# Performance work log

Measured on AMD Instinct MI355X. Metric: run time of the kernel, lower is better.

The kernel has to match this reference:

```python
import jax, jax.numpy as jnp
import numpy as np

N, VW, DW, VP, DP, H, M = 1024, 50000, 300, 50, 100, 512, 256


def _run_dir(x, Wih, Whh, b, reverse):
    # Single-direction LSTM over [n, in] -> [n, H]. PyTorch gate order i,f,g,o.
    Hh = Whh.shape[1]
    def step(carry, xt):
        h, c = carry
        z = xt @ Wih.T + h @ Whh.T + b  # [4H]
        i, f, g, o = jnp.split(z, 4, axis=-1)
        c = jax.nn.sigmoid(f) * c + jax.nn.sigmoid(i) * jnp.tanh(g)
        h = jax.nn.sigmoid(o) * jnp.tanh(c)
        return (h, c), h
    init = (jnp.zeros((Hh,), x.dtype), jnp.zeros((Hh,), x.dtype))
    _, hs = jax.lax.scan(step, init, x, reverse=reverse)
    return hs


def setup_inputs() -> dict:
    key = jax.random.key(0)
    ks = jax.random.split(key, 24)
    s = 0.05  # small init to keep tanh/sigmoid unsaturated
    d = {
        "word_idx": jax.random.randint(ks[0], (N,), 0, VW, dtype=jnp.int32),
        "pos_idx": jax.random.randint(ks[1], (N,), 0, VP, dtype=jnp.int32),
        "word_emb": jax.random.normal(ks[2], (VW, DW), jnp.float32) * s,
        "pos_emb": jax.random.normal(ks[3], (VP, DP), jnp.float32) * s,
        "wih0f": jax.random.normal(ks[4], (4 * H, DW + DP), jnp.float32) * s,
        "whh0f": jax.random.normal(ks[5], (4 * H, H), jnp.float32) * s,
        "b0f": jax.random.normal(ks[6], (4 * H,), jnp.float32) * s,
        "wih0r": jax.random.normal(ks[7], (4 * H, DW + DP), jnp.float32) * s,
        "whh0r": jax.random.normal(ks[8], (4 * H, H), jnp.float32) * s,
        "b0r": jax.random.normal(ks[9], (4 * H,), jnp.float32) * s,
        "wih1f": jax.random.normal(ks[10], (4 * H, 2 * H), jnp.float32) * s,
        "whh1f": jax.random.normal(ks[11], (4 * H, H), jnp.float32) * s,
        "b1f": jax.random.normal(ks[12], (4 * H,), jnp.float32) * s,
        "wih1r": jax.random.normal(ks[13], (4 * H, 2 * H), jnp.float32) * s,
        "whh1r": jax.random.normal(ks[14], (4 * H, H), jnp.float32) * s,
        "b1r": jax.random.normal(ks[15], (4 * H,), jnp.float32) * s,
        "W1": jax.random.normal(ks[16], (M, 4 * H), jnp.float32) * s,
        "bmlp1": jax.random.normal(ks[17], (M,), jnp.float32) * s,
        "w2": jax.random.normal(ks[18], (1, M), jnp.float32) * s,
        "b2": jax.random.normal(ks[19], (1,), jnp.float32) * s,
    }
    return d


def reference(word_idx, pos_idx, word_emb, pos_emb,
              wih0f, whh0f, b0f, wih0r, whh0r, b0r,
              wih1f, whh1f, b1f, wih1r, whh1r, b1r,
              W1, bmlp1, w2, b2):
    # Embed words + pos, concat -> [n, 400]
    x = jnp.concatenate([word_emb[word_idx], pos_emb[pos_idx]], axis=1)
    # 2-layer bidirectional LSTM encoder (batch of 1 squeezed away, as in the module)
    h0 = jnp.concatenate([_run_dir(x, wih0f, whh0f, b0f, False),
                          _run_dir(x, wih0r, whh0r, b0r, True)], axis=1)   # [n, 2H]
    h1 = jnp.concatenate([_run_dir(h0, wih1f, whh1f, b1f, False),
                          _run_dir(h0, wih1r, whh1r, b1r, True)], axis=1)  # [n, 2H]
    # Pairwise MLP score: MLP(concat(h_i, h_j)). Split W1 into head/dep halves so the
    # big GEMM is done once per token instead of once per pair (same math).
    twoH = h1.shape[1]
    a = h1 @ W1[:, :twoH].T            # [n, M], contribution of h_i
    bpart = h1 @ W1[:, twoH:].T        # [n, M], contribution of h_j
    hidden = jnp.tanh(a[:, None, :] + bpart[None, :, :] + bmlp1)  # [n, n, M]
    scores = hidden @ w2[0] + b2[0]    # [n, n]
    return scores
```

## Files before the change

### kernel.cpp

```cpp
#include <hip/hip_runtime.h>
#include <hip/hip_bf16.h>

#define HID   512
#define SEQ   1024
#define GATES 2048

__device__ __forceinline__ float sigm(float x) {
    return 1.f / (1.f + __expf(-x));
}
__device__ __forceinline__ float tanh_fast(float x) {
    float ax = fabsf(x);
    float e  = __expf(-2.f * ax);
    float t  = (1.f - e) * __builtin_amdgcn_rcpf(1.f + e);
    return copysignf(t, x);
}
__device__ __forceinline__ float bcast(float v, int l) {
    return __uint_as_float((unsigned)__builtin_amdgcn_readlane((int)__float_as_uint(v), l));
}

__global__ void embed_kernel(const int* __restrict__ wi, const int* __restrict__ pi,
                             const float* __restrict__ we, const float* __restrict__ pe,
                             float* __restrict__ x) {
    int i = blockIdx.x;
    int t = threadIdx.x;
    const float* w = we + (size_t)wi[i] * 300;
    const float* p = pe + (size_t)pi[i] * 100;
    float* xo = x + (size_t)i * 400;
    for (int c = t; c < 300; c += 128) xo[c]       = w[c];
    for (int c = t; c < 100; c += 128) xo[300 + c] = p[c];
}

__global__ __launch_bounds__(256)
void gemm_bias2(const float* __restrict__ A,
                const float* __restrict__ B0, const float* __restrict__ bias0, float* __restrict__ C0,
                const float* __restrict__ B1, const float* __restrict__ bias1, float* __restrict__ C1,
                int M, int N, int K, int lda, int ldb, int ldc) {
    const float* B    = blockIdx.z ? B1    : B0;
    const float* bias = blockIdx.z ? bias1 : bias0;
    float*       C    = blockIdx.z ? C1    : C0;

    __shared__ __align__(16) float As[16 * 132];
    __shared__ __align__(16) float Bs[16 * 68];
    const int tid  = threadIdx.x;
    const int bn   = blockIdx.x, bm = blockIdx.y;
    const int tj   = tid & 15, ti = tid >> 4;
    const int arow = tid >> 1;
    const int ak8  = (tid & 1) * 8;
    const int brow = tid >> 2;
    const int bk4  = (tid & 3) * 4;
    float acc[8][4] = {};

    for (int kt = 0; kt < K; kt += 16) {
        float4 a0 = *(const float4*)(A + (size_t)(bm * 128 + arow) * lda + kt + ak8);
        float4 a1 = *(const float4*)(A + (size_t)(bm * 128 + arow) * lda + kt + ak8 + 4);
        float4 bv = *(const float4*)(B + (size_t)(bn * 64 + brow) * ldb + kt + bk4);
        As[(ak8 + 0) * 132 + arow] = a0.x; As[(ak8 + 1) * 132 + arow] = a0.y;
        As[(ak8 + 2) * 132 + arow] = a0.z; As[(ak8 + 3) * 132 + arow] = a0.w;
        As[(ak8 + 4) * 132 + arow] = a1.x; As[(ak8 + 5) * 132 + arow] = a1.y;
        As[(ak8 + 6) * 132 + arow] = a1.z; As[(ak8 + 7) * 132 + arow] = a1.w;
        Bs[(bk4 + 0) * 68 + brow] = bv.x; Bs[(bk4 + 1) * 68 + brow] = bv.y;
        Bs[(bk4 + 2) * 68 + brow] = bv.z; Bs[(bk4 + 3) * 68 + brow] = bv.w;
        __syncthreads();
        #pragma unroll
        for (int k = 0; k < 16; ++k) {
            float4 x0 = *(const float4*)&As[k * 132 + ti * 8];
            float4 x1 = *(const float4*)&As[k * 132 + ti * 8 + 4];
            float4 b4 = *(const float4*)&Bs[k * 68 + tj * 4];
            const float av[8] = {x0.x, x0.y, x0.z, x0.w, x1.x, x1.y, x1.z, x1.w};
            #pragma unroll
            for (int i = 0; i < 8; ++i) {
                acc[i][0] = fmaf(av[i], b4.x, acc[i][0]);
                acc[i][1] = fmaf(av[i], b4.y, acc[i][1]);
                acc[i][2] = fmaf(av[i], b4.z, acc[i][2]);
                acc[i][3] = fmaf(av[i], b4.w, acc[i][3]);
            }
        }
        __syncthreads();
    }
    const int n0 = bn * 64 + tj * 4;
    float bb0 = 0.f, bb1 = 0.f, bb2 = 0.f, bb3 = 0.f;
    if (bias) { bb0 = bias[n0]; bb1 = bias[n0 + 1]; bb2 = bias[n0 + 2]; bb3 = bias[n0 + 3]; }
    #pragma unroll
    for (int i = 0; i < 8; ++i) {
        float4 o;
        o.x = acc[i][0] + bb0; o.y = acc[i][1] + bb1;
        o.z = acc[i][2] + bb2; o.w = acc[i][3] + bb3;
        *(float4*)(C + (size_t)(bm * 128 + ti * 8 + i) * ldc + n0) = o;
    }
}

__global__ __launch_bounds__(576)
void lstm_layer(const float* __restrict__ Zf, const float* __restrict__ Zr,
                const float* __restrict__ WhhF, const float* __restrict__ WhhR,
                unsigned long long* __restrict__ Hpair,
                float* __restrict__ Hout,
                unsigned tagBase) {
    const int dir = blockIdx.x >> 5;
    const int wg  = blockIdx.x & 31;
    const float* __restrict__ Z   = dir ? Zr   : Zf;
    const float* __restrict__ Whh = dir ? WhhR : WhhF;
    const int colOff = dir ? HID : 0;

    const int tid  = threadIdx.x;
    const int wave = tid >> 6;
    const int lane = tid & 63;
    const int g    = lane >> 4;
    const int jj   = lane & 15;
    const int grow = g * HID + wg * 16 + jj;

    __shared__ float part[2][8 * 65];

    if (wave == 0) {
        float cval = 0.f;
        float zin = Z[(size_t)(dir ? (SEQ - 1) : 0) * GATES + grow];
        for (int s = 0; s < SEQ; ++s) {
            const int t = dir ? (SEQ - 1 - s) : s;
            float znxt = 0.f;
            if (s + 1 < SEQ) {
                const int tn = dir ? (SEQ - 2 - s) : (s + 1);
                znxt = Z[(size_t)tn * GATES + grow];
            }
            __syncthreads();
            const float* pp = part[s & 1];
            float r = zin;
            #pragma unroll
            for (int c = 0; c < 8; ++c) r += pp[c * 65 + lane];
            float nl = (g == 2) ? tanh_fast(r) : sigm(r);
            float ig = __shfl(nl, jj);
            float fg = __shfl(nl, 16 + jj);
            float gg = __shfl(nl, 32 + jj);
            float og = __shfl(nl, 48 + jj);
            if (lane < 16) {
                cval = fg * cval + ig * gg;
                float hv = og * tanh_fast(cval);
                const size_t oidx = (size_t)t * (2 * HID) + colOff + wg * 16 + lane;
                unsigned long long pk = ((unsigned long long)(tagBase + (unsigned)s) << 32)
                                      | (unsigned long long)__float_as_uint(hv);
                __hip_atomic_store(Hpair + oidx, pk, __ATOMIC_RELAXED, __HIP_MEMORY_SCOPE_AGENT);
                Hout[oidx] = hv;
            }
            zin = znxt;
        }
    } else {
        const int kc = wave - 1;
        float w[64];
        {
            const float4* wp = (const float4*)(Whh + (size_t)grow * HID + kc * 64);
            #pragma unroll
            for (int q = 0; q < 16; ++q) {
                float4 v = wp[q];
                w[4 * q] = v.x; w[4 * q + 1] = v.y; w[4 * q + 2] = v.z; w[4 * q + 3] = v.w;
            }
        }
        for (int s = 0; s < SEQ; ++s) {
            const int t = dir ? (SEQ - 1 - s) : s;
            float acc = 0.f;
            if (s > 0) {
                const int tp = dir ? (t + 1) : (t - 1);
                const unsigned expTag = tagBase + (unsigned)s - 1u;
                const unsigned long long* hp =
                    Hpair + (size_t)tp * (2 * HID) + colOff + kc * 64 + lane;
                unsigned long long va, vb, v;
                va = __hip_atomic_load(hp, __ATOMIC_RELAXED, __HIP_MEMORY_SCOPE_AGENT);
                for (;;) {
                    vb = __hip_atomic_load(hp, __ATOMIC_RELAXED, __HIP_MEMORY_SCOPE_AGENT);
                    if (__all((unsigned)(va >> 32) == expTag)) { v = va; break; }
                    va = __hip_atomic_load(hp, __ATOMIC_RELAXED, __HIP_MEMORY_SCOPE_AGENT);
                    if (__all((unsigned)(vb >> 32) == expTag)) { v = vb; break; }
                }
                float hv = __uint_as_float((unsigned)v);
                float a0 = 0.f, a1 = 0.f, a2 = 0.f, a3 = 0.f;
                #pragma unroll
                for (int m = 0; m < 64; m += 4) {
                    a0 = fmaf(w[m + 0], bcast(hv, m + 0), a0);
                    a1 = fmaf(w[m + 1], bcast(hv, m + 1), a1);
                    a2 = fmaf(w[m + 2], bcast(hv, m + 2), a2);
                    a3 = fmaf(w[m + 3], bcast(hv, m + 3), a3);
                }
                acc = (a0 + a1) + (a2 + a3);
            }
            part[s & 1][kc * 65 + lane] = acc;
            __syncthreads();
        }
    }
}

__global__ __launch_bounds__(256)
void pairwise_kernel(const float* __restrict__ Ah, const float* __restrict__ Bd,
                     const float* __restrict__ w2, const float* __restrict__ b2,
                     float* __restrict__ out) {
    __shared__ __align__(16) float at[16 * 260];
    __shared__ __align__(16) float bt[16 * 260];
    __shared__ __align__(16) float wl[256];
    const int tid = threadIdx.x;
    const int i0 = blockIdx.y * 16, j0 = blockIdx.x * 16;
    for (int u = tid; u < 16 * 256; u += 256) {
        int r = u >> 8, m = u & 255;
        at[r * 260 + m] = Ah[(size_t)(i0 + r) * 256 + m];
        bt[r * 260 + m] = Bd[(size_t)(j0 + r) * 256 + m];
    }
    wl[tid] = w2[tid];
    __syncthreads();
    const int tj = tid & 15, ti = tid >> 4;
    float acc = b2[0];
    #pragma unroll 2
    for (int m = 0; m < 256; m += 4) {
        float4 a4 = *(const float4*)&at[ti * 260 + m];
        float4 b4 = *(const float4*)&bt[tj * 260 + m];
        float4 w4 = *(const float4*)&wl[m];
        acc += tanh_fast(a4.x + b4.x) * w4.x;
        acc += tanh_fast(a4.y + b4.y) * w4.y;
        acc += tanh_fast(a4.z + b4.z) * w4.z;
        acc += tanh_fast(a4.w + b4.w) * w4.w;
    }
    out[(size_t)(i0 + ti) * 1024 + (j0 + tj)] = acc;
}

extern "C" void kernel_launch(void* const* d_in, const int* in_sizes, int n_in,
                              void* d_out, int out_size, void* d_ws, size_t ws_size,
                              hipStream_t stream) {
    const int*   wi    = (const int*)  d_in[0];
    const int*   pi    = (const int*)  d_in[1];
    const float* we    = (const float*)d_in[2];
    const float* pe    = (const float*)d_in[3];
    const float* wih0f = (const float*)d_in[4];
    const float* whh0f = (const float*)d_in[5];
    const float* b0f   = (const float*)d_in[6];
    const float* wih0r = (const float*)d_in[7];
    const float* whh0r = (const float*)d_in[8];
    const float* b0r   = (const float*)d_in[9];
    const float* wih1f = (const float*)d_in[10];
    const float* whh1f = (const float*)d_in[11];
    const float* b1f   = (const float*)d_in[12];
    const float* wih1r = (const float*)d_in[13];
    const float* whh1r = (const float*)d_in[14];
    const float* b1r   = (const float*)d_in[15];
    const float* W1    = (const float*)d_in[16];
    const float* bmlp1 = (const float*)d_in[17];
    const float* w2    = (const float*)d_in[18];
    const float* b2    = (const float*)d_in[19];
    float* out = (float*)d_out;

    char* wsb = (char*)d_ws;
    float* x  = (float*)(wsb + 512);
    float* zA = x  + (size_t)1024 * 400;
    float* zB = zA + (size_t)1024 * 2048;
    float* h0 = zB + (size_t)1024 * 2048;
    float* h1 = h0 + (size_t)1024 * 1024;
    float* aH = h1 + (size_t)1024 * 1024;
    float* bD = aH + (size_t)1024 * 256;
    unsigned long long* Hpair = (unsigned long long*)(bD + (size_t)1024 * 256);

    embed_kernel<<<dim3(1024), dim3(128), 0, stream>>>(wi, pi, we, pe, x);

    gemm_bias2<<<dim3(32, 8, 2), dim3(256), 0, stream>>>(
        x, wih0f, b0f, zA, wih0r, b0r, zB, 1024, 2048, 400, 400, 400, 2048);

    lstm_layer<<<dim3(64), dim3(576), 0, stream>>>(zA, zB, whh0f, whh0r, Hpair, h0, 1u);

    gemm_bias2<<<dim3(32, 8, 2), dim3(256), 0, stream>>>(
        h0, wih1f, b1f, zA, wih1r, b1r, zB, 1024, 2048, 1024, 1024, 1024, 2048);

    lstm_layer<<<dim3(64), dim3(576), 0, stream>>>(zA, zB, whh1f, whh1r, Hpair, h1, 8192u);

    gemm_bias2<<<dim3(4, 8, 2), dim3(256), 0, stream>>>(
        h1, W1, bmlp1, aH, W1 + 1024, nullptr, bD, 1024, 256, 1024, 1024, 2048, 256);

    pairwise_kernel<<<dim3(64, 64), dim3(256), 0, stream>>>(aH, bD, w2, b2, out);
}
```

Baseline: 3.392 ms.

## Enlarge GEMM and pairwise tiles, pipeline LSTM spin-wait loads

The input-projection GEMM tile grows from 128x64 to 128x128, so each thread computes an 8x8 block and loads less shared memory per FMA. The pairwise scoring kernel moves to 32x32 tiles with 2x2 outputs per thread and an XOR-swizzled shared layout, reads w2 straight from global memory, and shares each A/B load across four tanh evaluations. The LSTM spin-wait now keeps three loads in flight as a rolling window instead of alternating two. The trade-off is higher register pressure and fewer blocks for the small GEMM, while the LSTM recurrence, which probably dominates runtime, is mostly unchanged.

```diff
diff --git a/kernel.cpp b/kernel.cpp
--- a/kernel.cpp
+++ b/kernel.cpp
@@ -31,61 +31,66 @@
 }
 
 __global__ __launch_bounds__(256)
-void gemm_bias2(const float* __restrict__ A,
-                const float* __restrict__ B0, const float* __restrict__ bias0, float* __restrict__ C0,
-                const float* __restrict__ B1, const float* __restrict__ bias1, float* __restrict__ C1,
-                int M, int N, int K, int lda, int ldb, int ldc) {
+void gemm128(const float* __restrict__ A,
+             const float* __restrict__ B0, const float* __restrict__ bias0, float* __restrict__ C0,
+             const float* __restrict__ B1, const float* __restrict__ bias1, float* __restrict__ C1,
+             int K, int lda, int ldb, int ldc) {
     const float* B    = blockIdx.z ? B1    : B0;
     const float* bias = blockIdx.z ? bias1 : bias0;
     float*       C    = blockIdx.z ? C1    : C0;
 
     __shared__ __align__(16) float As[16 * 132];
-    __shared__ __align__(16) float Bs[16 * 68];
+    __shared__ __align__(16) float Bs[16 * 132];
     const int tid  = threadIdx.x;
     const int bn   = blockIdx.x, bm = blockIdx.y;
     const int tj   = tid & 15, ti = tid >> 4;
-    const int arow = tid >> 1;
-    const int ak8  = (tid & 1) * 8;
-    const int brow = tid >> 2;
-    const int bk4  = (tid & 3) * 4;
-    float acc[8][4] = {};
+    const int row2 = tid >> 1;
+    const int k8   = (tid & 1) * 8;
+    float acc[8][8] = {};
 
     for (int kt = 0; kt < K; kt += 16) {
-        float4 a0 = *(const float4*)(A + (size_t)(bm * 128 + arow) * lda + kt + ak8);
-        float4 a1 = *(const float4*)(A + (size_t)(bm * 128 + arow) * lda + kt + ak8 + 4);
-        float4 bv = *(const float4*)(B + (size_t)(bn * 64 + brow) * ldb + kt + bk4);
-        As[(ak8 + 0) * 132 + arow] = a0.x; As[(ak8 + 1) * 132 + arow] = a0.y;
-        As[(ak8 + 2) * 132 + arow] = a0.z; As[(ak8 + 3) * 132 + arow] = a0.w;
-        As[(ak8 + 4) * 132 + arow] = a1.x; As[(ak8 + 5) * 132 + arow] = a1.y;
-        As[(ak8 + 6) * 132 + arow] = a1.z; As[(ak8 + 7) * 132 + arow] = a1.w;
-        Bs[(bk4 + 0) * 68 + brow] = bv.x; Bs[(bk4 + 1) * 68 + brow] = bv.y;
-        Bs[(bk4 + 2) * 68 + brow] = bv.z; Bs[(bk4 + 3) * 68 + brow] = bv.w;
+        float4 a0 = *(const float4*)(A + (size_t)(bm * 128 + row2) * lda + kt + k8);
+        float4 a1 = *(const float4*)(A + (size_t)(bm * 128 + row2) * lda + kt + k8 + 4);
+        float4 b0 = *(const float4*)(B + (size_t)(bn * 128 + row2) * ldb + kt + k8);
+        float4 b1 = *(const float4*)(B + (size_t)(bn * 128 + row2) * ldb + kt + k8 + 4);
+        As[(k8 + 0) * 132 + row2] = a0.x; As[(k8 + 1) * 132 + row2] = a0.y;
+        As[(k8 + 2) * 132 + row2] = a0.z; As[(k8 + 3) * 132 + row2] = a0.w;
+        As[(k8 + 4) * 132 + row2] = a1.x; As[(k8 + 5) * 132 + row2] = a1.y;
+        As[(k8 + 6) * 132 + row2] = a1.z; As[(k8 + 7) * 132 + row2] = a1.w;
+        Bs[(k8 + 0) * 132 + row2] = b0.x; Bs[(k8 + 1) * 132 + row2] = b0.y;
+        Bs[(k8 + 2) * 132 + row2] = b0.z; Bs[(k8 + 3) * 132 + row2] = b0.w;
+        Bs[(k8 + 4) * 132 + row2] = b1.x; Bs[(k8 + 5) * 132 + row2] = b1.y;
+        Bs[(k8 + 6) * 132 + row2] = b1.z; Bs[(k8 + 7) * 132 + row2] = b1.w;
         __syncthreads();
         #pragma unroll
         for (int k = 0; k < 16; ++k) {
             float4 x0 = *(const float4*)&As[k * 132 + ti * 8];
             float4 x1 = *(const float4*)&As[k * 132 + ti * 8 + 4];
-            float4 b4 = *(const float4*)&Bs[k * 68 + tj * 4];
+            float4 y0 = *(const float4*)&Bs[k * 132 + tj * 8];
+            float4 y1 = *(const float4*)&Bs[k * 132 + tj * 8 + 4];
             const float av[8] = {x0.x, x0.y, x0.z, x0.w, x1.x, x1.y, x1.z, x1.w};
+            const float bv[8] = {y0.x, y0.y, y0.z, y0.w, y1.x, y1.y, y1.z, y1.w};
             #pragma unroll
-            for (int i = 0; i < 8; ++i) {
-                acc[i][0] = fmaf(av[i], b4.x, acc[i][0]);
-                acc[i][1] = fmaf(av[i], b4.y, acc[i][1]);
-                acc[i][2] = fmaf(av[i], b4.z, acc[i][2]);
-                acc[i][3] = fmaf(av[i], b4.w, acc[i][3]);
-            }
+            for (int i = 0; i < 8; ++i)
+                #pragma unroll
+                for (int j = 0; j < 8; ++j)
+                    acc[i][j] = fmaf(av[i], bv[j], acc[i][j]);
         }
         __syncthreads();
     }
-    const int n0 = bn * 64 + tj * 4;
-    float bb0 = 0.f, bb1 = 0.f, bb2 = 0.f, bb3 = 0.f;
-    if (bias) { bb0 = bias[n0]; bb1 = bias[n0 + 1]; bb2 = bias[n0 + 2]; bb3 = bias[n0 + 3]; }
+    const int n0 = bn * 128 + tj * 8;
+    float bb[8];
+    #pragma unroll
+    for (int j = 0; j < 8; ++j) bb[j] = bias ? bias[n0 + j] : 0.f;
     #pragma unroll
     for (int i = 0; i < 8; ++i) {
-        float4 o;
-        o.x = acc[i][0] + bb0; o.y = acc[i][1] + bb1;
-        o.z = acc[i][2] + bb2; o.w = acc[i][3] + bb3;
-        *(float4*)(C + (size_t)(bm * 128 + ti * 8 + i) * ldc + n0) = o;
+        float4 o0, o1;
+        o0.x = acc[i][0] + bb[0]; o0.y = acc[i][1] + bb[1];
+        o0.z = acc[i][2] + bb[2]; o0.w = acc[i][3] + bb[3];
+        o1.x = acc[i][4] + bb[4]; o1.y = acc[i][5] + bb[5];
+        o1.z = acc[i][6] + bb[6]; o1.w = acc[i][7] + bb[7];
+        float* cp = C + (size_t)(bm * 128 + ti * 8 + i) * ldc + n0;
+        *(float4*)cp = o0; *(float4*)(cp + 4) = o1;
     }
 }
 
@@ -160,13 +165,13 @@
                 const unsigned expTag = tagBase + (unsigned)s - 1u;
                 const unsigned long long* hp =
                     Hpair + (size_t)tp * (2 * HID) + colOff + kc * 64 + lane;
-                unsigned long long va, vb, v;
+                unsigned long long va, vb, vc, v;
                 va = __hip_atomic_load(hp, __ATOMIC_RELAXED, __HIP_MEMORY_SCOPE_AGENT);
+                vb = __hip_atomic_load(hp, __ATOMIC_RELAXED, __HIP_MEMORY_SCOPE_AGENT);
                 for (;;) {
-                    vb = __hip_atomic_load(hp, __ATOMIC_RELAXED, __HIP_MEMORY_SCOPE_AGENT);
+                    vc = __hip_atomic_load(hp, __ATOMIC_RELAXED, __HIP_MEMORY_SCOPE_AGENT);
                     if (__all((unsigned)(va >> 32) == expTag)) { v = va; break; }
-                    va = __hip_atomic_load(hp, __ATOMIC_RELAXED, __HIP_MEMORY_SCOPE_AGENT);
-                    if (__all((unsigned)(vb >> 32) == expTag)) { v = vb; break; }
+                    va = vb; vb = vc;
                 }
                 float hv = __uint_as_float((unsigned)v);
                 float a0 = 0.f, a1 = 0.f, a2 = 0.f, a3 = 0.f;
@@ -189,31 +194,49 @@
 void pairwise_kernel(const float* __restrict__ Ah, const float* __restrict__ Bd,
                      const float* __restrict__ w2, const float* __restrict__ b2,
                      float* __restrict__ out) {
-    __shared__ __align__(16) float at[16 * 260];
-    __shared__ __align__(16) float bt[16 * 260];
-    __shared__ __align__(16) float wl[256];
+    __shared__ __align__(16) float at[32 * 256];
+    __shared__ __align__(16) float bt[32 * 256];
     const int tid = threadIdx.x;
-    const int i0 = blockIdx.y * 16, j0 = blockIdx.x * 16;
-    for (int u = tid; u < 16 * 256; u += 256) {
-        int r = u >> 8, m = u & 255;
-        at[r * 260 + m] = Ah[(size_t)(i0 + r) * 256 + m];
-        bt[r * 260 + m] = Bd[(size_t)(j0 + r) * 256 + m];
-    }
-    wl[tid] = w2[tid];
+    const int i0 = blockIdx.y * 32, j0 = blockIdx.x * 32;
+    for (int p = 0; p < 32; ++p) {
+        int m = tid;
+        int sw = ((m >> 2) ^ ((p >> 1) & 7)) * 4 + (m & 3);
+        at[p * 256 + sw] = Ah[(size_t)(i0 + p) * 256 + m];
+        bt[p * 256 + sw] = Bd[(size_t)(j0 + p) * 256 + m];
+    }
     __syncthreads();
     const int tj = tid & 15, ti = tid >> 4;
-    float acc = b2[0];
-    #pragma unroll 2
+    const int qa4 = (ti & 7) * 4;
+    const int qb4 = (tj & 7) * 4;
+    const float* a0p = &at[(2 * ti) * 256];
+    const float* a1p = a0p + 256;
+    const float* b0p = &bt[(2 * tj) * 256];
+    const float* b1p = b0p + 256;
+    const float bias = b2[0];
+    float acc00 = bias, acc01 = bias, acc10 = bias, acc11 = bias;
+    #pragma unroll 4
     for (int m = 0; m < 256; m += 4) {
-        float4 a4 = *(const float4*)&at[ti * 260 + m];
-        float4 b4 = *(const float4*)&bt[tj * 260 + m];
-        float4 w4 = *(const float4*)&wl[m];
-        acc += tanh_fast(a4.x + b4.x) * w4.x;
-        acc += tanh_fast(a4.y + b4.y) * w4.y;
-        acc += tanh_fast(a4.z + b4.z) * w4.z;
-        acc += tanh_fast(a4.w + b4.w) * w4.w;
-    }
-    out[(size_t)(i0 + ti) * 1024 + (j0 + tj)] = acc;
+        const int ca = m ^ qa4, cb = m ^ qb4;
+        float4 a0 = *(const float4*)&a0p[ca];
+        float4 a1 = *(const float4*)&a1p[ca];
+        float4 b0 = *(const float4*)&b0p[cb];
+        float4 b1 = *(const float4*)&b1p[cb];
+        float4 w4 = *(const float4*)&w2[m];
+        acc00 += tanh_fast(a0.x + b0.x) * w4.x; acc01 += tanh_fast(a0.x + b1.x) * w4.x;
+        acc10 += tanh_fast(a1.x + b0.x) * w4.x; acc11 += tanh_fast(a1.x + b1.x) * w4.x;
+        acc00 += tanh_fast(a0.y + b0.y) * w4.y; acc01 += tanh_fast(a0.y + b1.y) * w4.y;
+        acc10 += tanh_fast(a1.y + b0.y) * w4.y; acc11 += tanh_fast(a1.y + b1.y) * w4.y;
+        acc00 += tanh_fast(a0.z + b0.z) * w4.z; acc01 += tanh_fast(a0.z + b1.z) * w4.z;
+        acc10 += tanh_fast(a1.z + b0.z) * w4.z; acc11 += tanh_fast(a1.z + b1.z) * w4.z;
+        acc00 += tanh_fast(a0.w + b0.w) * w4.w; acc01 += tanh_fast(a0.w + b1.w) * w4.w;
+        acc10 += tanh_fast(a1.w + b0.w) * w4.w; acc11 += tanh_fast(a1.w + b1.w) * w4.w;
+    }
+    float* o0 = out + (size_t)(i0 + 2 * ti) * 1024 + j0 + 2 * tj;
+    float* o1 = o0 + 1024;
+    float2 r0; r0.x = acc00; r0.y = acc01;
+    float2 r1; r1.x = acc10; r1.y = acc11;
+    *(float2*)o0 = r0;
+    *(float2*)o1 = r1;
 }
 
 extern "C" void kernel_launch(void* const* d_in, const int* in_sizes, int n_in,
@@ -253,18 +276,18 @@
 
     embed_kernel<<<dim3(1024), dim3(128), 0, stream>>>(wi, pi, we, pe, x);
 
-    gemm_bias2<<<dim3(32, 8, 2), dim3(256), 0, stream>>>(
-        x, wih0f, b0f, zA, wih0r, b0r, zB, 1024, 2048, 400, 400, 400, 2048);
+    gemm128<<<dim3(16, 8, 2), dim3(256), 0, stream>>>(
+        x, wih0f, b0f, zA, wih0r, b0r, zB, 400, 400, 400, 2048);
 
     lstm_layer<<<dim3(64), dim3(576), 0, stream>>>(zA, zB, whh0f, whh0r, Hpair, h0, 1u);
 
-    gemm_bias2<<<dim3(32, 8, 2), dim3(256), 0, stream>>>(
-        h0, wih1f, b1f, zA, wih1r, b1r, zB, 1024, 2048, 1024, 1024, 1024, 2048);
+    gemm128<<<dim3(16, 8, 2), dim3(256), 0, stream>>>(
+        h0, wih1f, b1f, zA, wih1r, b1r, zB, 1024, 1024, 1024, 2048);
 
     lstm_layer<<<dim3(64), dim3(576), 0, stream>>>(zA, zB, whh1f, whh1r, Hpair, h1, 8192u);
 
-    gemm_bias2<<<dim3(4, 8, 2), dim3(256), 0, stream>>>(
-        h1, W1, bmlp1, aH, W1 + 1024, nullptr, bD, 1024, 256, 1024, 1024, 2048, 256);
-
-    pairwise_kernel<<<dim3(64, 64), dim3(256), 0, stream>>>(aH, bD, w2, b2, out);
-}
+    gemm128<<<dim3(2, 8, 2), dim3(256), 0, stream>>>(
+        h1, W1, bmlp1, aH, W1 + 1024, nullptr, bD, 1024, 1024, 2048, 256);
+
+    pairwise_kernel<<<dim3(32, 32), dim3(256), 0, stream>>>(aH, bD, w2, b2, out);
+}
```

Measured after the change: 3.950 ms. 1.16x slower.
